# Optimization experiments

Hardware: AMD Instinct MI355X
Metric: run time of the kernel (lower is better)

## Reference

```python
import jax, jax.numpy as jnp
import numpy as np

FACTOR = 5

def setup_inputs() -> dict:
    key = jax.random.key(0)
    k1, k2, k3, k4 = jax.random.split(key, 4)
    B, L, E = 64, 4096, 64
    sample_k = min(FACTOR * int(np.ceil(np.log(L))), L)  # 45
    return {
        "queries": jax.random.normal(k1, (B, L, E), dtype=jnp.float32),
        "keys": jax.random.normal(k2, (B, L, E), dtype=jnp.float32),
        "values": jax.random.normal(k3, (B, L, E), dtype=jnp.float32),
        "index_sample": jax.random.randint(k4, (L, sample_k), 0, L, dtype=jnp.int32),
    }

def reference(queries, keys, values, index_sample):
    B, L_Q, D = queries.shape
    _, L_K, _ = keys.shape
    u = min(FACTOR * int(np.ceil(np.log(L_Q))), L_Q)  # n_top queries

    # --- _prob_QK: random K-sample gather + sparsity measure + topk ---
    # K_sample: (B, L_Q, sample_k, E) via gather (no dense K_expand materialized)
    K_sample = keys[:, index_sample, :]
    Q_K_sample = jnp.einsum('ble,blse->bls', queries, K_sample)
    M = Q_K_sample.max(-1) - Q_K_sample.sum(-1) / L_K  # (B, L_Q)
    _, M_top = jax.lax.top_k(M, u)  # (B, u) indices of top queries

    Q_reduce = jnp.take_along_axis(queries, M_top[:, :, None], axis=1)  # (B, u, E)
    scores_top = jnp.einsum('bue,bke->buk', Q_reduce, keys)  # (B, u, L_K)

    scale = 1.0 / np.sqrt(D)
    scores_top = scores_top * scale

    # --- _get_initial_context: mask_flag=True -> cumulative sum of V ---
    context = jnp.cumsum(values, axis=-2)  # (B, L_Q, D)

    # --- _update_context: softmax over full keys, scatter into context rows ---
    attn = jax.nn.softmax(scores_top, axis=-1)  # (B, u, L_K)
    upd = jnp.einsum('buk,bkd->bud', attn, values)  # (B, u, D)
    context = context.at[jnp.arange(B)[:, None], M_top, :].set(upd)
    return context
```

## Files before the change

### kernel.cpp

```cpp
#include <hip/hip_runtime.h>

#define Bv 64
#define Lv 4096
#define Dv 64
#define Uv 45
#define UP 48
#define NC 16
#define CKK 256
#define NSUB 64

#define OFF_M    0
#define SZ_M     (Bv*Lv)
#define OFF_QR   (OFF_M + SZ_M)
#define SZ_QR    (Bv*UP*Dv)
#define OFF_PMS  (OFF_QR + SZ_QR)
#define SZ_PMS   (Bv*NC*2*UP)
#define OFF_DEN  (OFF_PMS + SZ_PMS)
#define SZ_DEN   (Bv*2*UP)
#define OFF_PPV  (OFF_DEN + SZ_DEN)
#define SZ_PPV   (Bv*NC*UP*Dv)
#define OFF_CS   (OFF_PPV + SZ_PPV)
#define SZ_CS    (Bv*NSUB*Dv)
#define OFF_TOP  (OFF_CS + SZ_CS)
#define SZ_TOP   (Bv*Uv)

__global__ __launch_bounds__(256) void k_M(const float* __restrict__ Q,
                                           const float* __restrict__ K,
                                           const int* __restrict__ idx,
                                           float* __restrict__ Mout) {
  __shared__ int sidx[32 * Uv];
  int i = blockIdx.x;
  int x = i & 7, j = i >> 3;
  int b = x + 8 * (j >> 7);
  int w = j & 127;
  int t = threadIdx.x;
  for (int p = t; p < 32 * Uv; p += 256) sidx[p] = idx[(w * 32) * Uv + p];
  int g = t >> 3, lane = t & 7;
  int l = w * 32 + g;
  const float4* qr = (const float4*)(Q + ((size_t)b * Lv + l) * Dv + lane * 8);
  float4 q0 = qr[0], q1 = qr[1];
  const char* Kb = (const char*)(K + (size_t)b * Lv * Dv) + lane * 32;
  __syncthreads();
  float mx = -3.0e38f, sm = 0.f;
#pragma unroll 3
  for (int s = 0; s < Uv; s++) {
    int ki = sidx[g * Uv + s];
    const float4* kr = (const float4*)(Kb + (size_t)ki * 256);
    float4 k0 = kr[0], k1 = kr[1];
    float d = q0.x * k0.x + q0.y * k0.y + q0.z * k0.z + q0.w * k0.w
            + q1.x * k1.x + q1.y * k1.y + q1.z * k1.z + q1.w * k1.w;
    d += __shfl_xor(d, 1);
    d += __shfl_xor(d, 2);
    d += __shfl_xor(d, 4);
    mx = fmaxf(mx, d);
    sm += d;
  }
  if (lane == 0) Mout[(size_t)b * Lv + l] = mx - sm * (1.0f / (float)Lv);
}

__global__ __launch_bounds__(1024) void k_topk(const float* __restrict__ M,
                                               const float* __restrict__ Q,
                                               int* __restrict__ Mtop,
                                               float* __restrict__ Qr) {
  __shared__ float wv[16];
  __shared__ int wi[16];
  __shared__ float win_v;
  __shared__ int win_i;
  __shared__ int list[Uv];
  int b = blockIdx.x;
  int t = threadIdx.x;
  const float* Mb = M + (size_t)b * Lv;
  float r0 = Mb[t], r1 = Mb[t + 1024], r2 = Mb[t + 2048], r3 = Mb[t + 3072];
  int wave = t >> 6, lane = t & 63;
  for (int it = 0; it < Uv; it++) {
    float bv = r0; int bi = t;
    if (r1 > bv) { bv = r1; bi = t + 1024; }
    if (r2 > bv) { bv = r2; bi = t + 2048; }
    if (r3 > bv) { bv = r3; bi = t + 3072; }
#pragma unroll
    for (int off = 1; off < 64; off <<= 1) {
      float v2 = __shfl_xor(bv, off);
      int i2 = __shfl_xor(bi, off);
      if (v2 > bv || (v2 == bv && i2 < bi)) { bv = v2; bi = i2; }
    }
    if (lane == 0) { wv[wave] = bv; wi[wave] = bi; }
    __syncthreads();
    if (t < 64) {
      float cv = (lane < 16) ? wv[lane] : -3.0e38f;
      int ci = (lane < 16) ? wi[lane] : (1 << 30);
#pragma unroll
      for (int off = 1; off < 16; off <<= 1) {
        float v2 = __shfl_xor(cv, off);
        int i2 = __shfl_xor(ci, off);
        if (v2 > cv || (v2 == cv && i2 < ci)) { cv = v2; ci = i2; }
      }
      if (lane == 0) { win_v = cv; win_i = ci; list[it] = ci; }
    }
    __syncthreads();
    int wn = win_i;
    if ((wn & 1023) == t) {
      int c = wn >> 10;
      if (c == 0) r0 = -3.0e38f;
      else if (c == 1) r1 = -3.0e38f;
      else if (c == 2) r2 = -3.0e38f;
      else r3 = -3.0e38f;
    }
    __syncthreads();
  }
  if (t < Uv) Mtop[b * Uv + t] = list[t];
  for (int p = t; p < UP * Dv; p += 1024) {
    int u = p >> 6, e = p & 63;
    float v = 0.f;
    if (u < Uv) {
      int row = list[u];
      v = Q[((size_t)b * Lv + row) * Dv + e] * 0.125f;
    }
    Qr[((size_t)b * UP + u) * Dv + e] = v;
  }
}

#define STAGE_QST(QS, QR, b)                                        \
  for (int i_ = threadIdx.x; i_ < Dv * UP; i_ += blockDim.x) {      \
    int u_ = i_ >> 6, e_ = i_ & 63;                                 \
    QS[e_ * UP + u_] = QR[((size_t)(b) * UP + u_) * Dv + e_];       \
  }

#define SCORE_TILE(ACC, QS, KMAT, b_, c_, ug_, kg_)                                   \
  {                                                                                    \
    const float* Kb_ = (KMAT) + ((size_t)(b_) * Lv + (size_t)(c_) * CKK + (kg_)) * Dv; \
    for (int e = 0; e < Dv; e += 4) {                                                  \
      float qq[4][8];                                                                  \
      _Pragma("unroll")                                                                \
      for (int e2 = 0; e2 < 4; e2++) {                                                 \
        float4 qa = *(const float4*)&(QS)[(e + e2) * UP + (ug_) * 8];                  \
        float4 qb = *(const float4*)&(QS)[(e + e2) * UP + (ug_) * 8 + 4];              \
        qq[e2][0]=qa.x; qq[e2][1]=qa.y; qq[e2][2]=qa.z; qq[e2][3]=qa.w;                \
        qq[e2][4]=qb.x; qq[e2][5]=qb.y; qq[e2][6]=qb.z; qq[e2][7]=qb.w;                \
      }                                                                                \
      _Pragma("unroll")                                                                \
      for (int j = 0; j < 8; j++) {                                                    \
        float4 kv = *(const float4*)(Kb_ + (size_t)(32 * j) * Dv + e);                 \
        _Pragma("unroll")                                                              \
        for (int uu = 0; uu < 8; uu++)                                                 \
          ACC[uu][j] += qq[0][uu]*kv.x + qq[1][uu]*kv.y + qq[2][uu]*kv.z + qq[3][uu]*kv.w; \
      }                                                                                  \
    }                                                                                  \
  }

__global__ __launch_bounds__(192) void k_ms(const float* __restrict__ Kmat,
                                            const float* __restrict__ Qr,
                                            float* __restrict__ pms) {
  __shared__ float qsT[Dv * UP];
  int b = blockIdx.x >> 4, c = blockIdx.x & 15;
  STAGE_QST(qsT, Qr, b);
  __syncthreads();
  int t = threadIdx.x, ug = t >> 5, kg = t & 31;
  float acc[8][8];
#pragma unroll
  for (int uu = 0; uu < 8; uu++)
#pragma unroll
    for (int j = 0; j < 8; j++) acc[uu][j] = 0.f;
  SCORE_TILE(acc, qsT, Kmat, b, c, ug, kg);
#pragma unroll
  for (int uu = 0; uu < 8; uu++) {
    float m = acc[uu][0];
#pragma unroll
    for (int j = 1; j < 8; j++) m = fmaxf(m, acc[uu][j]);
#pragma unroll
    for (int off = 1; off < 32; off <<= 1) m = fmaxf(m, __shfl_xor(m, off));
    float s = 0.f;
#pragma unroll
    for (int j = 0; j < 8; j++) s += __expf(acc[uu][j] - m);
#pragma unroll
    for (int off = 1; off < 32; off <<= 1) s += __shfl_xor(s, off);
    if (kg == 0) {
      pms[(((size_t)b * NC + c) * 2 + 0) * UP + ug * 8 + uu] = m;
      pms[(((size_t)b * NC + c) * 2 + 1) * UP + ug * 8 + uu] = s;
    }
  }
}

__global__ __launch_bounds__(64) void k_den(const float* __restrict__ pms,
                                            float* __restrict__ den) {
  int b = blockIdx.x, u = threadIdx.x;
  if (u >= UP) return;
  float mx = -3.0e38f;
  for (int c = 0; c < NC; c++)
    mx = fmaxf(mx, pms[(((size_t)b * NC + c) * 2 + 0) * UP + u]);
  float d = 0.f;
  for (int c = 0; c < NC; c++)
    d += pms[(((size_t)b * NC + c) * 2 + 1) * UP + u] *
         __expf(pms[(((size_t)b * NC + c) * 2 + 0) * UP + u] - mx);
  den[(size_t)b * 2 * UP + u] = mx;
  den[(size_t)b * 2 * UP + UP + u] = 1.f / d;
}

__global__ __launch_bounds__(192) void k_pv(const float* __restrict__ Kmat,
                                            const float* __restrict__ V,
                                            const float* __restrict__ Qr,
                                            const float* __restrict__ den,
                                            float* __restrict__ ppv) {
  __shared__ float qsT[Dv * UP];
  __shared__ float wl[UP * CKK];
  int b = blockIdx.x >> 4, c = blockIdx.x & 15;
  STAGE_QST(qsT, Qr, b);
  __syncthreads();
  int t = threadIdx.x, ug = t >> 5, kg = t & 31;
  {
    float acc[8][8];
#pragma unroll
    for (int uu = 0; uu < 8; uu++)
#pragma unroll
      for (int j = 0; j < 8; j++) acc[uu][j] = 0.f;
    SCORE_TILE(acc, qsT, Kmat, b, c, ug, kg);
#pragma unroll
    for (int uu = 0; uu < 8; uu++) {
      float mx = den[(size_t)b * 2 * UP + ug * 8 + uu];
      float iv = den[(size_t)b * 2 * UP + UP + ug * 8 + uu];
#pragma unroll
      for (int j = 0; j < 8; j++)
        wl[(ug * 8 + uu) * CKK + kg + 32 * j] = __expf(acc[uu][j] - mx) * iv;
    }
  }
  __syncthreads();
  int w = t >> 6, lane = t & 63;
  float acc2[16];
#pragma unroll
  for (int uu = 0; uu < 16; uu++) acc2[uu] = 0.f;
  const float* Vb = V + ((size_t)b * Lv + (size_t)c * CKK) * Dv;
  for (int k4 = 0; k4 < CKK; k4 += 4) {
    float v0 = Vb[(size_t)(k4 + 0) * Dv + lane];
    float v1 = Vb[(size_t)(k4 + 1) * Dv + lane];
    float v2 = Vb[(size_t)(k4 + 2) * Dv + lane];
    float v3 = Vb[(size_t)(k4 + 3) * Dv + lane];
#pragma unroll
    for (int uu = 0; uu < 16; uu++) {
      float4 w4 = *(const float4*)&wl[(w * 16 + uu) * CKK + k4];
      acc2[uu] += w4.x * v0 + w4.y * v1 + w4.z * v2 + w4.w * v3;
    }
  }
#pragma unroll
  for (int uu = 0; uu < 16; uu++)
    ppv[(((size_t)b * NC + c) * UP + w * 16 + uu) * Dv + lane] = acc2[uu];
}

__global__ __launch_bounds__(256) void k_cs1(const float* __restrict__ V,
                                             float* __restrict__ cs) {
  int b = blockIdx.x >> 4, c4 = blockIdx.x & 15;
  int g = threadIdx.x >> 6, d = threadIdx.x & 63;
  int sub = c4 * 4 + g;
  const float* Vb = V + ((size_t)b * Lv + sub * 64) * Dv + d;
  float acc = 0.f;
  for (int r = 0; r < 64; r++) acc += Vb[(size_t)r * Dv];
  cs[((size_t)b * NSUB + sub) * Dv + d] = acc;
}

__global__ __launch_bounds__(256) void k_cs3(const float* __restrict__ V,
                                             const float* __restrict__ cs,
                                             float* __restrict__ out) {
  int b = blockIdx.x >> 4, c4 = blockIdx.x & 15;
  int g = threadIdx.x >> 6, d = threadIdx.x & 63;
  int sub = c4 * 4 + g;
  float acc = 0.f;
  for (int s = 0; s < sub; s++) acc += cs[((size_t)b * NSUB + s) * Dv + d];
  const float* Vb = V + ((size_t)b * Lv + sub * 64) * Dv + d;
  float* Ob = out + ((size_t)b * Lv + sub * 64) * Dv + d;
  for (int r = 0; r < 64; r++) {
    acc += Vb[(size_t)r * Dv];
    Ob[(size_t)r * Dv] = acc;
  }
}

__global__ __launch_bounds__(64) void k_upd(const float* __restrict__ ppv,
                                            const int* __restrict__ Mtop,
                                            float* __restrict__ out) {
  int b = blockIdx.x / Uv, u = blockIdx.x % Uv;
  int d = threadIdx.x;
  float s = 0.f;
  for (int c = 0; c < NC; c++)
    s += ppv[(((size_t)b * NC + c) * UP + u) * Dv + d];
  int row = Mtop[b * Uv + u];
  out[((size_t)b * Lv + row) * Dv + d] = s;
}

extern "C" void kernel_launch(void* const* d_in, const int* in_sizes, int n_in,
                              void* d_out, int out_size, void* d_ws, size_t ws_size,
                              hipStream_t stream) {
  (void)in_sizes; (void)n_in; (void)out_size; (void)ws_size;
  const float* Q = (const float*)d_in[0];
  const float* K = (const float*)d_in[1];
  const float* V = (const float*)d_in[2];
  const int* idx = (const int*)d_in[3];
  float* out = (float*)d_out;
  float* wsf = (float*)d_ws;
  float* M   = wsf + OFF_M;
  float* Qr  = wsf + OFF_QR;
  float* pms = wsf + OFF_PMS;
  float* den = wsf + OFF_DEN;
  float* ppv = wsf + OFF_PPV;
  float* cs  = wsf + OFF_CS;
  int* top   = (int*)(wsf + OFF_TOP);

  k_M<<<8192, 256, 0, stream>>>(Q, K, idx, M);
  k_topk<<<Bv, 1024, 0, stream>>>(M, Q, top, Qr);
  k_ms<<<Bv * NC, 192, 0, stream>>>(K, Qr, pms);
  k_den<<<Bv, 64, 0, stream>>>(pms, den);
  k_pv<<<Bv * NC, 192, 0, stream>>>(K, V, Qr, den, ppv);
  k_cs1<<<1024, 256, 0, stream>>>(V, cs);
  k_cs3<<<1024, 256, 0, stream>>>(V, cs, out);
  k_upd<<<Bv * Uv, 64, 0, stream>>>(ppv, top, out);
}
```

Before: 596.3 us.

## Halve key chunk size, pad Q tile, and reduce PV partials with atomics

The key chunk per block drops from 256 to 128, doubling the grid of the score and PV kernels to 2048 blocks and halving per-thread accumulators. The per-chunk PV partials are now summed into a zeroed buffer with float atomicAdd, which removes the large ppv partial buffer and the loop over chunks in the update kernel. The transposed Q tile in LDS gains a padded stride to reduce bank conflicts. This adds a zeroing kernel and atomic contention, and float atomics make the summation order nondeterministic.

```diff
diff --git a/kernel.cpp b/kernel.cpp
--- a/kernel.cpp
+++ b/kernel.cpp
@@ -5,8 +5,10 @@
 #define Dv 64
 #define Uv 45
 #define UP 48
-#define NC 16
-#define CKK 256
+#define NC 32
+#define CKK 128
+#define NJ 4
+#define UPP 52
 #define NSUB 64
 
 #define OFF_M    0
@@ -17,9 +19,9 @@
 #define SZ_PMS   (Bv*NC*2*UP)
 #define OFF_DEN  (OFF_PMS + SZ_PMS)
 #define SZ_DEN   (Bv*2*UP)
-#define OFF_PPV  (OFF_DEN + SZ_DEN)
-#define SZ_PPV   (Bv*NC*UP*Dv)
-#define OFF_CS   (OFF_PPV + SZ_PPV)
+#define OFF_UPD  (OFF_DEN + SZ_DEN)
+#define SZ_UPD   (Bv*UP*Dv)
+#define OFF_CS   (OFF_UPD + SZ_UPD)
 #define SZ_CS    (Bv*NSUB*Dv)
 #define OFF_TOP  (OFF_CS + SZ_CS)
 #define SZ_TOP   (Bv*Uv)
@@ -64,8 +66,7 @@
                                                float* __restrict__ Qr) {
   __shared__ float wv[16];
   __shared__ int wi[16];
-  __shared__ float win_v;
-  __shared__ int win_i;
+  __shared__ int win_i_s;
   __shared__ int list[Uv];
   int b = blockIdx.x;
   int t = threadIdx.x;
@@ -94,10 +95,10 @@
         int i2 = __shfl_xor(ci, off);
         if (v2 > cv || (v2 == cv && i2 < ci)) { cv = v2; ci = i2; }
       }
-      if (lane == 0) { win_v = cv; win_i = ci; list[it] = ci; }
+      if (lane == 0) { win_i_s = ci; list[it] = ci; }
     }
     __syncthreads();
-    int wn = win_i;
+    int wn = win_i_s;
     if ((wn & 1023) == t) {
       int c = wn >> 10;
       if (c == 0) r0 = -3.0e38f;
@@ -122,7 +123,7 @@
 #define STAGE_QST(QS, QR, b)                                        \
   for (int i_ = threadIdx.x; i_ < Dv * UP; i_ += blockDim.x) {      \
     int u_ = i_ >> 6, e_ = i_ & 63;                                 \
-    QS[e_ * UP + u_] = QR[((size_t)(b) * UP + u_) * Dv + e_];       \
+    QS[e_ * UPP + u_] = QR[((size_t)(b) * UP + u_) * Dv + e_];      \
   }
 
 #define SCORE_TILE(ACC, QS, KMAT, b_, c_, ug_, kg_)                                   \
@@ -132,45 +133,45 @@
       float qq[4][8];                                                                  \
       _Pragma("unroll")                                                                \
       for (int e2 = 0; e2 < 4; e2++) {                                                 \
-        float4 qa = *(const float4*)&(QS)[(e + e2) * UP + (ug_) * 8];                  \
-        float4 qb = *(const float4*)&(QS)[(e + e2) * UP + (ug_) * 8 + 4];              \
+        float4 qa = *(const float4*)&(QS)[(e + e2) * UPP + (ug_) * 8];                 \
+        float4 qb = *(const float4*)&(QS)[(e + e2) * UPP + (ug_) * 8 + 4];             \
         qq[e2][0]=qa.x; qq[e2][1]=qa.y; qq[e2][2]=qa.z; qq[e2][3]=qa.w;                \
         qq[e2][4]=qb.x; qq[e2][5]=qb.y; qq[e2][6]=qb.z; qq[e2][7]=qb.w;                \
       }                                                                                \
       _Pragma("unroll")                                                                \
-      for (int j = 0; j < 8; j++) {                                                    \
+      for (int j = 0; j < NJ; j++) {                                                   \
         float4 kv = *(const float4*)(Kb_ + (size_t)(32 * j) * Dv + e);                 \
         _Pragma("unroll")                                                              \
         for (int uu = 0; uu < 8; uu++)                                                 \
           ACC[uu][j] += qq[0][uu]*kv.x + qq[1][uu]*kv.y + qq[2][uu]*kv.z + qq[3][uu]*kv.w; \
-      }                                                                                  \
+      }                                                                                \
     }                                                                                  \
   }
 
 __global__ __launch_bounds__(192) void k_ms(const float* __restrict__ Kmat,
                                             const float* __restrict__ Qr,
                                             float* __restrict__ pms) {
-  __shared__ float qsT[Dv * UP];
-  int b = blockIdx.x >> 4, c = blockIdx.x & 15;
+  __shared__ float qsT[Dv * UPP];
+  int b = blockIdx.x >> 5, c = blockIdx.x & 31;
   STAGE_QST(qsT, Qr, b);
   __syncthreads();
   int t = threadIdx.x, ug = t >> 5, kg = t & 31;
-  float acc[8][8];
+  float acc[8][NJ];
 #pragma unroll
   for (int uu = 0; uu < 8; uu++)
 #pragma unroll
-    for (int j = 0; j < 8; j++) acc[uu][j] = 0.f;
+    for (int j = 0; j < NJ; j++) acc[uu][j] = 0.f;
   SCORE_TILE(acc, qsT, Kmat, b, c, ug, kg);
 #pragma unroll
   for (int uu = 0; uu < 8; uu++) {
     float m = acc[uu][0];
 #pragma unroll
-    for (int j = 1; j < 8; j++) m = fmaxf(m, acc[uu][j]);
+    for (int j = 1; j < NJ; j++) m = fmaxf(m, acc[uu][j]);
 #pragma unroll
     for (int off = 1; off < 32; off <<= 1) m = fmaxf(m, __shfl_xor(m, off));
     float s = 0.f;
 #pragma unroll
-    for (int j = 0; j < 8; j++) s += __expf(acc[uu][j] - m);
+    for (int j = 0; j < NJ; j++) s += __expf(acc[uu][j] - m);
 #pragma unroll
     for (int off = 1; off < 32; off <<= 1) s += __shfl_xor(s, off);
     if (kg == 0) {
@@ -195,30 +196,34 @@
   den[(size_t)b * 2 * UP + UP + u] = 1.f / d;
 }
 
+__global__ __launch_bounds__(256) void k_zero(float4* __restrict__ upd4) {
+  upd4[blockIdx.x * 256 + threadIdx.x] = make_float4(0.f, 0.f, 0.f, 0.f);
+}
+
 __global__ __launch_bounds__(192) void k_pv(const float* __restrict__ Kmat,
                                             const float* __restrict__ V,
                                             const float* __restrict__ Qr,
                                             const float* __restrict__ den,
-                                            float* __restrict__ ppv) {
-  __shared__ float qsT[Dv * UP];
+                                            float* __restrict__ upd) {
+  __shared__ float qsT[Dv * UPP];
   __shared__ float wl[UP * CKK];
-  int b = blockIdx.x >> 4, c = blockIdx.x & 15;
+  int b = blockIdx.x >> 5, c = blockIdx.x & 31;
   STAGE_QST(qsT, Qr, b);
   __syncthreads();
   int t = threadIdx.x, ug = t >> 5, kg = t & 31;
   {
-    float acc[8][8];
+    float acc[8][NJ];
 #pragma unroll
     for (int uu = 0; uu < 8; uu++)
 #pragma unroll
-      for (int j = 0; j < 8; j++) acc[uu][j] = 0.f;
+      for (int j = 0; j < NJ; j++) acc[uu][j] = 0.f;
     SCORE_TILE(acc, qsT, Kmat, b, c, ug, kg);
 #pragma unroll
     for (int uu = 0; uu < 8; uu++) {
       float mx = den[(size_t)b * 2 * UP + ug * 8 + uu];
       float iv = den[(size_t)b * 2 * UP + UP + ug * 8 + uu];
 #pragma unroll
-      for (int j = 0; j < 8; j++)
+      for (int j = 0; j < NJ; j++)
         wl[(ug * 8 + uu) * CKK + kg + 32 * j] = __expf(acc[uu][j] - mx) * iv;
     }
   }
@@ -241,7 +246,7 @@
   }
 #pragma unroll
   for (int uu = 0; uu < 16; uu++)
-    ppv[(((size_t)b * NC + c) * UP + w * 16 + uu) * Dv + lane] = acc2[uu];
+    atomicAdd(&upd[((size_t)b * UP + w * 16 + uu) * Dv + lane], acc2[uu]);
 }
 
 __global__ __launch_bounds__(256) void k_cs1(const float* __restrict__ V,
@@ -271,14 +276,12 @@
   }
 }
 
-__global__ __launch_bounds__(64) void k_upd(const float* __restrict__ ppv,
+__global__ __launch_bounds__(64) void k_upd(const float* __restrict__ upd,
                                             const int* __restrict__ Mtop,
                                             float* __restrict__ out) {
   int b = blockIdx.x / Uv, u = blockIdx.x % Uv;
   int d = threadIdx.x;
-  float s = 0.f;
-  for (int c = 0; c < NC; c++)
-    s += ppv[(((size_t)b * NC + c) * UP + u) * Dv + d];
+  float s = upd[((size_t)b * UP + u) * Dv + d];
   int row = Mtop[b * Uv + u];
   out[((size_t)b * Lv + row) * Dv + d] = s;
 }
@@ -297,7 +300,7 @@
   float* Qr  = wsf + OFF_QR;
   float* pms = wsf + OFF_PMS;
   float* den = wsf + OFF_DEN;
-  float* ppv = wsf + OFF_PPV;
+  float* upd = wsf + OFF_UPD;
   float* cs  = wsf + OFF_CS;
   int* top   = (int*)(wsf + OFF_TOP);
 
@@ -305,8 +308,9 @@
   k_topk<<<Bv, 1024, 0, stream>>>(M, Q, top, Qr);
   k_ms<<<Bv * NC, 192, 0, stream>>>(K, Qr, pms);
   k_den<<<Bv, 64, 0, stream>>>(pms, den);
-  k_pv<<<Bv * NC, 192, 0, stream>>>(K, V, Qr, den, ppv);
+  k_zero<<<(Bv * UP * Dv) / 1024, 256, 0, stream>>>((float4*)upd);
+  k_pv<<<Bv * NC, 192, 0, stream>>>(K, V, Qr, den, upd);
   k_cs1<<<1024, 256, 0, stream>>>(V, cs);
   k_cs3<<<1024, 256, 0, stream>>>(V, cs, out);
-  k_upd<<<Bv * Uv, 64, 0, stream>>>(ppv, top, out);
-}
+  k_upd<<<Bv * Uv, 64, 0, stream>>>(upd, top, out);
+}
```

Result: faster. 575.5 us (-3.5%).
